# Kernel optimization log

Hardware: AMD Instinct MI355X
Metric: run time of the kernel (lower is better)

The kernel has to match this reference:

```python
import jax, jax.numpy as jnp
import numpy as np

N_NODES = 8192
DIM = 512

def setup_inputs() -> dict:
    key = jax.random.key(0)
    k1, k2, k3, k4 = jax.random.split(key, 4)
    x = jax.random.normal(k1, (N_NODES, DIM), dtype=jnp.float32)
    adj = jax.random.uniform(k2, (N_NODES, N_NODES), dtype=jnp.float32)
    # nn.Linear(dim, dim): weight [out, in], bias [out]
    bound = 1.0 / np.sqrt(DIM)
    W = jax.random.uniform(k3, (DIM, DIM), minval=-bound, maxval=bound, dtype=jnp.float32)
    b = jax.random.uniform(k4, (DIM,), minval=-bound, maxval=bound, dtype=jnp.float32)
    return {"x": x, "adj": adj, "W": W, "b": b}

def reference(x, adj, W, b):
    # agg = adj @ x : [N, dim]
    agg = jnp.matmul(adj, x)
    # Linear: agg @ W.T + b, then ReLU
    out = jnp.matmul(agg, W.T) + b
    return jax.nn.relu(out)
```

## Files before the change

kernel.cpp:

```cpp
#include <hip/hip_runtime.h>

typedef __bf16 bf16_t;
typedef bf16_t bf16x8 __attribute__((ext_vector_type(8)));
typedef bf16_t bf16x4 __attribute__((ext_vector_type(4)));
typedef float f32x4 __attribute__((ext_vector_type(4)));

#define N_NODES 8192
#define DIM 512

__global__ __launch_bounds__(256) void k_transpose_x(const float* __restrict__ x,
                                                     bf16_t* __restrict__ xT) {
  __shared__ float tile[64][65];
  const int m0 = blockIdx.x * 64;
  const int n0 = blockIdx.y * 64;
  const int t = threadIdx.x;
  const int r = t >> 4;
  const int c = (t & 15) << 2;
#pragma unroll
  for (int i = 0; i < 4; ++i) {
    f32x4 v = *(const f32x4*)&x[(size_t)(m0 + r + i * 16) * DIM + n0 + c];
    tile[r + i * 16][c + 0] = v.x;
    tile[r + i * 16][c + 1] = v.y;
    tile[r + i * 16][c + 2] = v.z;
    tile[r + i * 16][c + 3] = v.w;
  }
  __syncthreads();
#pragma unroll
  for (int i = 0; i < 4; ++i) {
    const int rn = r + i * 16;
    bf16x4 o = {(bf16_t)tile[c + 0][rn], (bf16_t)tile[c + 1][rn],
                (bf16_t)tile[c + 2][rn], (bf16_t)tile[c + 3][rn]};
    *(bf16x4*)&xT[(size_t)(n0 + rn) * N_NODES + m0 + c] = o;
  }
}

__global__ __launch_bounds__(256) void k_cvt_w(const float* __restrict__ W,
                                               bf16_t* __restrict__ Wb) {
  const int t = blockIdx.x * 256 + threadIdx.x;
  f32x4 v = *(const f32x4*)&W[(size_t)t * 4];
  bf16x4 o = {(bf16_t)v.x, (bf16_t)v.y, (bf16_t)v.z, (bf16_t)v.w};
  *(bf16x4*)&Wb[(size_t)t * 4] = o;
}

template <int S>
__global__ __launch_bounds__(512, 4) void k_gemm1(const float* __restrict__ A,
                                                  const bf16_t* __restrict__ Bt,
                                                  float* __restrict__ P) {
  constexpr int K = N_NODES;
  constexpr int KC = K / S;
  constexpr int NIT = KC / 32;
  constexpr int LD = 40;
  __shared__ bf16_t As[2][128 * LD];
  __shared__ bf16_t Bs[2][128 * LD];

  const int b = blockIdx.x;
  const int xcd = b & 7;
  const int i6 = b >> 3;
  const int n_tile = i6 & 3;
  const int s = (i6 >> 2) & (S - 1);
  const int mg = (i6 >> 2) / S;
  const int m0 = (mg * 8 + xcd) * 128;
  const int n0 = n_tile * 128;

  const int t = threadIdx.x;
  const int lane = t & 63;
  const int w = t >> 6;
  const int wr = w & 1;
  const int wc = w >> 1;
  const int lrow = lane & 15;
  const int quad = lane >> 4;
  const int sr = t >> 2;
  const int sq = t & 3;

  const float* ap = A + (size_t)(m0 + sr) * K + s * KC + sq * 8;
  const bf16_t* bp = Bt + (size_t)(n0 + sr) * K + s * KC + sq * 8;
  const int wofs = sr * LD + sq * 8;

  f32x4 pa0[2], pa1[2];
  bf16x8 pb[2];
  auto load_pre = [&](int k0, int sl) {
    pa0[sl] = *(const f32x4*)(ap + k0);
    pa1[sl] = *(const f32x4*)(ap + k0 + 4);
    pb[sl] = *(const bf16x8*)(bp + k0);
  };
  auto stage = [&](int sl, int buf) {
    bf16x8 av;
#pragma unroll
    for (int z = 0; z < 4; ++z) {
      av[z] = (bf16_t)pa0[sl][z];
      av[z + 4] = (bf16_t)pa1[sl][z];
    }
    *(bf16x8*)&As[buf][wofs] = av;
    *(bf16x8*)&Bs[buf][wofs] = pb[sl];
  };

  load_pre(0, 0);
  stage(0, 0);
  if (NIT > 1) load_pre(32, 1);
  f32x4 acc[4][2] = {};
  __syncthreads();

  int cur = 0;
#pragma unroll 2
  for (int it = 0; it < NIT; ++it) {
    if (it + 2 < NIT) load_pre((it + 2) * 32, it & 1);
    bf16x8 af[4], bfr[2];
#pragma unroll
    for (int ii = 0; ii < 4; ++ii)
      af[ii] = *(const bf16x8*)&As[cur][(wr * 64 + ii * 16 + lrow) * LD + quad * 8];
#pragma unroll
    for (int jj = 0; jj < 2; ++jj)
      bfr[jj] = *(const bf16x8*)&Bs[cur][(wc * 32 + jj * 16 + lrow) * LD + quad * 8];
#pragma unroll
    for (int ii = 0; ii < 4; ++ii)
#pragma unroll
      for (int jj = 0; jj < 2; ++jj)
        acc[ii][jj] = __builtin_amdgcn_mfma_f32_16x16x32_bf16(af[ii], bfr[jj], acc[ii][jj], 0, 0, 0);
    if (it + 1 < NIT) stage((it + 1) & 1, cur ^ 1);
    __syncthreads();
    cur ^= 1;
  }

  float* Pp = P + (size_t)s * N_NODES * DIM;
#pragma unroll
  for (int ii = 0; ii < 4; ++ii)
#pragma unroll
    for (int jj = 0; jj < 2; ++jj) {
      const int col = n0 + wc * 32 + jj * 16 + lrow;
#pragma unroll
      for (int r = 0; r < 4; ++r) {
        const int row = m0 + wr * 64 + ii * 16 + quad * 4 + r;
        Pp[(size_t)row * DIM + col] = acc[ii][jj][r];
      }
    }
}

template <int S>
__global__ __launch_bounds__(256, 2) void k_gemm2(const float* __restrict__ P,
                                                  const bf16_t* __restrict__ Bw,
                                                  const float* __restrict__ bias,
                                                  float* __restrict__ out) {
  constexpr int K = DIM;
  constexpr int LDA = 72;
  constexpr int LDB = 72;
  constexpr size_t PS = (size_t)N_NODES * DIM;
  __shared__ bf16_t As[64 * LDA];
  __shared__ bf16_t Bs[128 * LDB];

  const int b = blockIdx.x;
  const int n0 = (b & 3) * 128;
  const int m0 = (b >> 2) * 64;
  const int t = threadIdx.x;
  const int lane = t & 63;
  const int w = t >> 6;
  const int wr = w & 1;
  const int wc = w >> 1;
  const int lrow = lane & 15;
  const int quad = lane >> 4;
  const int ar = t >> 2, aq = t & 3;
  const int br = t >> 1, bq = t & 1;

  const float* ap = P + (size_t)(m0 + ar) * K + aq * 16;
  const bf16_t* bp = Bw + (size_t)(n0 + br) * K + bq * 32;
  bf16_t* aw = &As[ar * LDA + aq * 16];
  bf16_t* bw = &Bs[br * LDB + bq * 32];

  f32x4 acc[2][4] = {};

  for (int k0 = 0; k0 < K; k0 += 64) {
    f32x4 av[4];
#pragma unroll
    for (int z = 0; z < 4; ++z) av[z] = *(const f32x4*)(ap + k0 + z * 4);
#pragma unroll
    for (int s2 = 1; s2 < S; ++s2)
#pragma unroll
      for (int z = 0; z < 4; ++z) av[z] += *(const f32x4*)(ap + s2 * PS + k0 + z * 4);
    bf16x8 b0 = *(const bf16x8*)(bp + k0);
    bf16x8 b1 = *(const bf16x8*)(bp + k0 + 8);
    bf16x8 b2 = *(const bf16x8*)(bp + k0 + 16);
    bf16x8 b3 = *(const bf16x8*)(bp + k0 + 24);
    bf16x8 a0, a1;
#pragma unroll
    for (int z = 0; z < 4; ++z) {
      a0[z] = (bf16_t)av[0][z];
      a0[z + 4] = (bf16_t)av[1][z];
      a1[z] = (bf16_t)av[2][z];
      a1[z + 4] = (bf16_t)av[3][z];
    }
    __syncthreads();
    *(bf16x8*)aw = a0;
    *(bf16x8*)(aw + 8) = a1;
    *(bf16x8*)bw = b0;
    *(bf16x8*)(bw + 8) = b1;
    *(bf16x8*)(bw + 16) = b2;
    *(bf16x8*)(bw + 24) = b3;
    __syncthreads();
#pragma unroll
    for (int kk = 0; kk < 64; kk += 32) {
      bf16x8 af0 = *(const bf16x8*)&As[(wr * 32 + 0 + lrow) * LDA + kk + quad * 8];
      bf16x8 af1 = *(const bf16x8*)&As[(wr * 32 + 16 + lrow) * LDA + kk + quad * 8];
      bf16x8 bf0 = *(const bf16x8*)&Bs[(wc * 64 + 0 + lrow) * LDB + kk + quad * 8];
      bf16x8 bf1 = *(const bf16x8*)&Bs[(wc * 64 + 16 + lrow) * LDB + kk + quad * 8];
      bf16x8 bf2 = *(const bf16x8*)&Bs[(wc * 64 + 32 + lrow) * LDB + kk + quad * 8];
      bf16x8 bf3 = *(const bf16x8*)&Bs[(wc * 64 + 48 + lrow) * LDB + kk + quad * 8];
      acc[0][0] = __builtin_amdgcn_mfma_f32_16x16x32_bf16(af0, bf0, acc[0][0], 0, 0, 0);
      acc[0][1] = __builtin_amdgcn_mfma_f32_16x16x32_bf16(af0, bf1, acc[0][1], 0, 0, 0);
      acc[0][2] = __builtin_amdgcn_mfma_f32_16x16x32_bf16(af0, bf2, acc[0][2], 0, 0, 0);
      acc[0][3] = __builtin_amdgcn_mfma_f32_16x16x32_bf16(af0, bf3, acc[0][3], 0, 0, 0);
      acc[1][0] = __builtin_amdgcn_mfma_f32_16x16x32_bf16(af1, bf0, acc[1][0], 0, 0, 0);
      acc[1][1] = __builtin_amdgcn_mfma_f32_16x16x32_bf16(af1, bf1, acc[1][1], 0, 0, 0);
      acc[1][2] = __builtin_amdgcn_mfma_f32_16x16x32_bf16(af1, bf2, acc[1][2], 0, 0, 0);
      acc[1][3] = __builtin_amdgcn_mfma_f32_16x16x32_bf16(af1, bf3, acc[1][3], 0, 0, 0);
    }
  }

#pragma unroll
  for (int i = 0; i < 2; ++i)
#pragma unroll
    for (int j = 0; j < 4; ++j) {
      const int col = n0 + wc * 64 + j * 16 + lrow;
      const float bj = bias[col];
#pragma unroll
      for (int r = 0; r < 4; ++r) {
        const int row = m0 + wr * 32 + i * 16 + quad * 4 + r;
        float v = acc[i][j][r] + bj;
        out[(size_t)row * DIM + col] = v > 0.0f ? v : 0.0f;
      }
    }
}

extern "C" void kernel_launch(void* const* d_in, const int* in_sizes, int n_in,
                              void* d_out, int out_size, void* d_ws, size_t ws_size,
                              hipStream_t stream) {
  const float* x = (const float*)d_in[0];
  const float* adj = (const float*)d_in[1];
  const float* W = (const float*)d_in[2];
  const float* b = (const float*)d_in[3];
  float* out = (float*)d_out;

  bf16_t* xT = (bf16_t*)d_ws;
  bf16_t* Wb = xT + (size_t)DIM * N_NODES;
  float* P = (float*)(Wb + (size_t)DIM * DIM);
  const size_t base = (size_t)DIM * N_NODES * 2 + (size_t)DIM * DIM * 2;
  const size_t pslab = (size_t)N_NODES * DIM * 4;

  k_transpose_x<<<dim3(N_NODES / 64, DIM / 64), 256, 0, stream>>>(x, xT);
  k_cvt_w<<<dim3((DIM * DIM / 4) / 256), 256, 0, stream>>>(W, Wb);

  if (ws_size >= base + 4 * pslab) {
    k_gemm1<4><<<dim3(256 * 4), 512, 0, stream>>>(adj, xT, P);
    k_gemm2<4><<<dim3(512), 256, 0, stream>>>(P, Wb, b, out);
  } else {
    k_gemm1<1><<<dim3(256), 512, 0, stream>>>(adj, xT, P);
    k_gemm2<1><<<dim3(512), 256, 0, stream>>>(P, Wb, b, out);
  }
}
```

Measured before the change: 508.1 us.

## Load B fragments directly from global into registers and swizzle A shared tile

The first GEMM no longer stages the bf16 B operand through shared memory. Each wave loads its B fragments straight from global memory into registers, double-buffered two iterations ahead. The A tile drops its padding in favour of an XOR swizzle, is prefetched four iterations deep, and the wave layout changes to 4x2 waves, each computing a 32x64 subtile. This is meant to cut LDS traffic and shared-memory footprint, at the cost of more registers, redundant global B loads across waves, and uncoalesced per-row B reads.

```diff
diff --git a/kernel.cpp b/kernel.cpp
--- a/kernel.cpp
+++ b/kernel.cpp
@@ -49,9 +49,7 @@
   constexpr int K = N_NODES;
   constexpr int KC = K / S;
   constexpr int NIT = KC / 32;
-  constexpr int LD = 40;
-  __shared__ bf16_t As[2][128 * LD];
-  __shared__ bf16_t Bs[2][128 * LD];
+  __shared__ bf16_t As[2][128 * 32];
 
   const int b = blockIdx.x;
   const int xcd = b & 7;
@@ -65,25 +63,33 @@
   const int t = threadIdx.x;
   const int lane = t & 63;
   const int w = t >> 6;
-  const int wr = w & 1;
-  const int wc = w >> 1;
+  const int wr = w >> 1;
+  const int wc = w & 1;
   const int lrow = lane & 15;
   const int quad = lane >> 4;
+  const int pg = quad ^ (lrow & 3);
+
   const int sr = t >> 2;
   const int sq = t & 3;
+  const int wofs = sr * 32 + ((sq ^ (sr & 3)) * 8);
 
   const float* ap = A + (size_t)(m0 + sr) * K + s * KC + sq * 8;
-  const bf16_t* bp = Bt + (size_t)(n0 + sr) * K + s * KC + sq * 8;
-  const int wofs = sr * LD + sq * 8;
-
-  f32x4 pa0[2], pa1[2];
-  bf16x8 pb[2];
-  auto load_pre = [&](int k0, int sl) {
+  const bf16_t* bp = Bt + (size_t)s * KC + quad * 8;
+  const int brow0 = n0 + wc * 64 + lrow;
+
+  f32x4 pa0[4], pa1[4];
+  bf16x8 bs[2][4];
+
+  auto loadA = [&](int k0, int sl) {
     pa0[sl] = *(const f32x4*)(ap + k0);
     pa1[sl] = *(const f32x4*)(ap + k0 + 4);
-    pb[sl] = *(const bf16x8*)(bp + k0);
-  };
-  auto stage = [&](int sl, int buf) {
+  };
+  auto loadB = [&](int k0, int sl) {
+#pragma unroll
+    for (int jj = 0; jj < 4; ++jj)
+      bs[sl][jj] = *(const bf16x8*)(bp + (size_t)(brow0 + jj * 16) * K + k0);
+  };
+  auto stageA = [&](int sl, int buf) {
     bf16x8 av;
 #pragma unroll
     for (int z = 0; z < 4; ++z) {
@@ -91,45 +97,51 @@
       av[z + 4] = (bf16_t)pa1[sl][z];
     }
     *(bf16x8*)&As[buf][wofs] = av;
-    *(bf16x8*)&Bs[buf][wofs] = pb[sl];
-  };
-
-  load_pre(0, 0);
-  stage(0, 0);
-  if (NIT > 1) load_pre(32, 1);
-  f32x4 acc[4][2] = {};
+  };
+
+  loadA(0, 0);
+  loadA(32, 1);
+  loadA(64, 2);
+  loadA(96, 3);
+  loadB(0, 0);
+  loadB(32, 1);
+  stageA(0, 0);
+  f32x4 acc[2][4] = {};
   __syncthreads();
 
   int cur = 0;
-#pragma unroll 2
-  for (int it = 0; it < NIT; ++it) {
-    if (it + 2 < NIT) load_pre((it + 2) * 32, it & 1);
-    bf16x8 af[4], bfr[2];
-#pragma unroll
-    for (int ii = 0; ii < 4; ++ii)
-      af[ii] = *(const bf16x8*)&As[cur][(wr * 64 + ii * 16 + lrow) * LD + quad * 8];
-#pragma unroll
-    for (int jj = 0; jj < 2; ++jj)
-      bfr[jj] = *(const bf16x8*)&Bs[cur][(wc * 32 + jj * 16 + lrow) * LD + quad * 8];
-#pragma unroll
-    for (int ii = 0; ii < 4; ++ii)
-#pragma unroll
-      for (int jj = 0; jj < 2; ++jj)
-        acc[ii][jj] = __builtin_amdgcn_mfma_f32_16x16x32_bf16(af[ii], bfr[jj], acc[ii][jj], 0, 0, 0);
-    if (it + 1 < NIT) stage((it + 1) & 1, cur ^ 1);
+  auto body = [&](int it, int sa, int sb, int snext) {
+    if (it + 4 < NIT) loadA((it + 4) * 32, sa);
+    const int rbase = wr * 32 + lrow;
+    bf16x8 af0 = *(const bf16x8*)&As[cur][(rbase + 0) * 32 + pg * 8];
+    bf16x8 af1 = *(const bf16x8*)&As[cur][(rbase + 16) * 32 + pg * 8];
+#pragma unroll
+    for (int jj = 0; jj < 4; ++jj) {
+      acc[0][jj] = __builtin_amdgcn_mfma_f32_16x16x32_bf16(af0, bs[sb][jj], acc[0][jj], 0, 0, 0);
+      acc[1][jj] = __builtin_amdgcn_mfma_f32_16x16x32_bf16(af1, bs[sb][jj], acc[1][jj], 0, 0, 0);
+    }
+    if (it + 2 < NIT) loadB((it + 2) * 32, sb);
+    if (it + 1 < NIT) stageA(snext, cur ^ 1);
     __syncthreads();
     cur ^= 1;
+  };
+
+  for (int it4 = 0; it4 < NIT; it4 += 4) {
+    body(it4 + 0, 0, 0, 1);
+    body(it4 + 1, 1, 1, 2);
+    body(it4 + 2, 2, 0, 3);
+    body(it4 + 3, 3, 1, 0);
   }
 
   float* Pp = P + (size_t)s * N_NODES * DIM;
 #pragma unroll
-  for (int ii = 0; ii < 4; ++ii)
-#pragma unroll
-    for (int jj = 0; jj < 2; ++jj) {
-      const int col = n0 + wc * 32 + jj * 16 + lrow;
+  for (int ii = 0; ii < 2; ++ii)
+#pragma unroll
+    for (int jj = 0; jj < 4; ++jj) {
+      const int col = n0 + wc * 64 + jj * 16 + lrow;
 #pragma unroll
       for (int r = 0; r < 4; ++r) {
-        const int row = m0 + wr * 64 + ii * 16 + quad * 4 + r;
+        const int row = m0 + wr * 32 + ii * 16 + quad * 4 + r;
         Pp[(size_t)row * DIM + col] = acc[ii][jj][r];
       }
     }
```

After: 652.1 us. 1.28x slower.
